# Performance work log

Measured on AMD Instinct MI355X. Metric: run time of the kernel, lower is better.

## Reference

```python
import jax, jax.numpy as jnp
import numpy as np

HIDDEN = 1024
N_HEADS = 16
HEAD_DIM = HIDDEN // N_HEADS  # 64
B, N = 2, 2048
SCALE = HIDDEN ** (-0.5)  # NOTE: original scales by full hidden_size, not head_dim


def setup_inputs() -> dict:
    key = jax.random.key(0)
    k1, k2 = jax.random.split(key)
    hidden_states = jax.random.normal(k1, (B, N, HIDDEN), dtype=jnp.float32)
    attention_mask = jnp.ones((B, N), dtype=jnp.int32)
    # per-head no-bias Linear(hidden -> 3*head_dim), stacked: [h, hidden, 3*head_dim]
    W_qkv = jax.random.normal(k2, (N_HEADS, HIDDEN, 3 * HEAD_DIM), dtype=jnp.float32) * (HIDDEN ** -0.5)
    return {"hidden_states": hidden_states, "attention_mask": attention_mask, "W_qkv": W_qkv}


def reference(hidden_states, attention_mask, W_qkv):
    # qkv: [b, h, n, 3*d]
    qkv = jnp.einsum('bnD,hDe->bhne', hidden_states, W_qkv)
    q, k, v = jnp.split(qkv, 3, axis=-1)  # each [b, h, n, d]
    scores = jnp.einsum('bhid,bhjd->bhij', q, k) * SCALE
    mask = attention_mask[:, None, None, :] == 0  # [b,1,1,n]
    scores = jnp.where(mask, -jnp.inf, scores)
    attn = jax.nn.softmax(scores, axis=-1)
    out = jnp.einsum('bhij,bhjd->bhid', attn, v)  # [b, h, n, d]
    # rearrange 'b h n d -> b n (h d)'
    return jnp.transpose(out, (0, 2, 1, 3)).reshape(out.shape[0], out.shape[2], -1)
```

## Files before the change

### kernel.cpp

```cpp
#include <hip/hip_runtime.h>
#include <hip/hip_bf16.h>


#define NH   16
#define HD   64
#define SEQ  2048
#define HID  1024
#define E3   192
#define QSCALE 0.04508422017f
#define MBIAS  -43.2808512f

typedef __attribute__((ext_vector_type(8))) short short8;
typedef __attribute__((ext_vector_type(4))) float f32x4;
typedef __attribute__((ext_vector_type(16))) float f32x16;
typedef unsigned short ushort_t;

#define MFMA16(a, b, c) __builtin_amdgcn_mfma_f32_16x16x32_bf16((a), (b), (c), 0, 0, 0)
#define MFMA32(a, b, c) __builtin_amdgcn_mfma_f32_32x32x16_bf16((a), (b), (c), 0, 0, 0)

#if __has_builtin(__builtin_amdgcn_exp2f)
#define EXP2(x) __builtin_amdgcn_exp2f(x)
#else
#define EXP2(x) exp2f(x)
#endif

static __device__ __forceinline__ ushort_t f2bf(float x) {
    unsigned u = __builtin_bit_cast(unsigned, x);
    unsigned r = u + 0x7fff + ((u >> 16) & 1);
    return (ushort_t)(r >> 16);
}

static __device__ __forceinline__ unsigned pack_trunc(float hi, float lo) {
#if __has_builtin(__builtin_amdgcn_perm)
    return __builtin_amdgcn_perm(__builtin_bit_cast(unsigned, hi),
                                 __builtin_bit_cast(unsigned, lo), 0x07060302u);
#else
    return (__builtin_bit_cast(unsigned, hi) & 0xffff0000u) |
           (__builtin_bit_cast(unsigned, lo) >> 16);
#endif
}

static __device__ __forceinline__ void load_lds16(const void* g, void* l) {
    __builtin_amdgcn_global_load_lds(
        (__attribute__((address_space(1))) void*)(g),
        (__attribute__((address_space(3))) void*)(l), 16, 0, 0);
}

__global__ __launch_bounds__(256) void k_cvt(const void* __restrict__ Xv,
                                             const void* __restrict__ Wv,
                                             ushort_t* __restrict__ Xb,
                                             ushort_t* __restrict__ Wt,
                                             int* __restrict__ flagp) {
    __shared__ int cnt;
    __shared__ ushort_t tile[64][72];
    const int t = threadIdx.x;
    if (threadIdx.x == 0) cnt = 0;
    __syncthreads();

    if (blockIdx.x < 1024) {
        const unsigned* X32 = (const unsigned*)Xv;
        if (t < 64) {
            unsigned u = X32[(size_t)blockIdx.x * 2048 + t * 32 + 7];
            int bexp = (u >> 7) & 0xFF;
            if (bexp >= 0x68 && bexp <= 0x90) atomicAdd(&cnt, 1);
        }
        __syncthreads();
        const int isf32 = (cnt < 32);
        if (blockIdx.x == 0 && t == 0) *flagp = isf32;

        const size_t base = ((size_t)blockIdx.x * 256 + t) * 16;
        if (isf32) {
            const float* Xf = (const float*)Xv;
            ushort_t tmp[16];
#pragma unroll
            for (int c = 0; c < 4; ++c) {
                float4 v = *(const float4*)(Xf + base + c * 4);
                tmp[c * 4 + 0] = f2bf(v.x); tmp[c * 4 + 1] = f2bf(v.y);
                tmp[c * 4 + 2] = f2bf(v.z); tmp[c * 4 + 3] = f2bf(v.w);
            }
            *(float4*)(Xb + base)     = ((const float4*)tmp)[0];
            *(float4*)(Xb + base + 8) = ((const float4*)tmp)[1];
        } else {
            const ushort_t* Xh = (const ushort_t*)Xv;
            *(float4*)(Xb + base)     = *(const float4*)(Xh + base);
            *(float4*)(Xb + base + 8) = *(const float4*)(Xh + base + 8);
        }
    } else {
        const int wb = blockIdx.x - 1024;
        const unsigned* W32 = (const unsigned*)Wv;
        if (t < 64) {
            unsigned u = W32[(size_t)wb * 2048 + t * 32 + 7];
            int bexp = (u >> 7) & 0xFF;
            if (bexp >= 0x68 && bexp <= 0x90) atomicAdd(&cnt, 1);
        }
        __syncthreads();
        const int isf32 = (cnt < 32);

        const int h  = wb & 15;
        const int dt = (wb >> 4) & 15;
        const int et = wb >> 8;
        const int D0 = dt * 64, e0 = et * 64;
#pragma unroll
        for (int r = 0; r < 2; ++r) {
            int row = r * 32 + (t >> 3);
            int col = (t & 7) * 8;
            size_t base = ((size_t)(h * HID + D0 + row)) * E3 + e0 + col;
            if (isf32) {
                const float* Wf = (const float*)Wv;
                float4 a = *(const float4*)(Wf + base);
                float4 c = *(const float4*)(Wf + base + 4);
                tile[row][col + 0] = f2bf(a.x); tile[row][col + 1] = f2bf(a.y);
                tile[row][col + 2] = f2bf(a.z); tile[row][col + 3] = f2bf(a.w);
                tile[row][col + 4] = f2bf(c.x); tile[row][col + 5] = f2bf(c.y);
                tile[row][col + 6] = f2bf(c.z); tile[row][col + 7] = f2bf(c.w);
            } else {
                *(float4*)&tile[row][col] = *(const float4*)((const ushort_t*)Wv + base);
            }
        }
        __syncthreads();
#pragma unroll
        for (int r = 0; r < 2; ++r) {
            int erow = r * 32 + (t >> 3);
            int dcol = (t & 7) * 8;
            ushort_t vals[8];
#pragma unroll
            for (int i = 0; i < 8; ++i) vals[i] = tile[dcol + i][erow];
            *(float4*)(Wt + ((size_t)(h * E3 + e0 + erow)) * HID + D0 + dcol) = *(float4*)vals;
        }
    }
}

__global__ __launch_bounds__(256) void k_qkv(const ushort_t* __restrict__ Xb,
                                             const ushort_t* __restrict__ Wt,
                                             ushort_t* __restrict__ Qb,
                                             ushort_t* __restrict__ Kb,
                                             ushort_t* __restrict__ Vtb) {
    __shared__ __align__(16) ushort_t smem[2 * 128 * 64];
    ushort_t* Xl = smem;
    ushort_t* Wl = smem + 128 * 64;

    const int bid = blockIdx.y * 24 + blockIdx.x;
    const int xcd = bid & 7, pos = bid >> 3;
    const int e0 = (xcd * 3 + (pos >> 5)) * 128;
    const int m0 = (pos & 31) * 128;
    const int b  = m0 >> 11;
    const int n0 = m0 & 2047;
    const int t = threadIdx.x;
    const int w = t >> 6, lane = t & 63, l15 = lane & 15, quad = lane >> 4;
    const int wrow0 = (w & 1) * 64, wcol0 = (w >> 1) * 64;
    const int srow = lane >> 3;
    const int scb  = (lane & 7) ^ srow;

    f32x4 acc[4][4];
#pragma unroll
    for (int i = 0; i < 4; ++i)
#pragma unroll
        for (int j = 0; j < 4; ++j) acc[i][j] = (f32x4){0.f, 0.f, 0.f, 0.f};

    for (int k0 = 0; k0 < HID; k0 += 64) {
        __syncthreads();
#pragma unroll
        for (int cc = 0; cc < 4; ++cc) {
            const int ch  = w * 4 + cc;
            const int row = ch * 8 + srow;
            load_lds16(Xb + (size_t)(m0 + row) * HID + k0 + scb * 8, &Xl[ch * 512]);
            load_lds16(Wt + (size_t)(e0 + row) * HID + k0 + scb * 8, &Wl[ch * 512]);
        }
        __syncthreads();
#pragma unroll
        for (int kh = 0; kh < 2; ++kh) {
            short8 af[4], bfm[4];
#pragma unroll
            for (int i = 0; i < 4; ++i) {
                const int r = wrow0 + i * 16 + l15;
                af[i] = *(const short8*)&Xl[r * 64 + ((kh * 4 + quad) ^ (r & 7)) * 8];
            }
#pragma unroll
            for (int j = 0; j < 4; ++j) {
                const int r = wcol0 + j * 16 + l15;
                bfm[j] = *(const short8*)&Wl[r * 64 + ((kh * 4 + quad) ^ (r & 7)) * 8];
            }
#pragma unroll
            for (int i = 0; i < 4; ++i)
#pragma unroll
                for (int j = 0; j < 4; ++j)
                    acc[i][j] = MFMA16(af[i], bfm[j], acc[i][j]);
        }
    }

    __syncthreads();
#pragma unroll
    for (int p = 0; p < 2; ++p) {
        const int E0  = e0 + p * 64;
        const int hh  = E0 / 192;
        const int r0p = E0 - hh * 192;
        const int own = ((w >> 1) == p);
        if (r0p < 128) {
            if (own) {
                const float sc = (r0p == 0) ? QSCALE : 1.0f;
#pragma unroll
                for (int i = 0; i < 4; ++i)
#pragma unroll
                    for (int j = 0; j < 4; ++j)
#pragma unroll
                        for (int reg = 0; reg < 4; ++reg)
                            smem[(wrow0 + i * 16 + quad * 4 + reg) * 72 + j * 16 + l15] =
                                f2bf(acc[i][j][reg] * sc);
            }
            __syncthreads();
            ushort_t* dstb = (r0p == 0) ? Qb : Kb;
            const int r = t >> 1, part = t & 1;
            size_t dst = ((size_t)(b * NH + hh) * SEQ + n0 + r) * HD + part * 32;
#pragma unroll
            for (int c = 0; c < 4; ++c)
                *(float4*)(dstb + dst + c * 8) = *(const float4*)&smem[r * 72 + part * 32 + c * 8];
        } else {
            if (own) {
#pragma unroll
                for (int i = 0; i < 4; ++i)
#pragma unroll
                    for (int j = 0; j < 4; ++j)
#pragma unroll
                        for (int reg = 0; reg < 4; ++reg)
                            smem[(j * 16 + l15) * 136 + wrow0 + i * 16 + quad * 4 + reg] =
                                f2bf(acc[i][j][reg]);
            }
            __syncthreads();
            const int dr = t >> 2, part = t & 3;
            size_t dst = ((size_t)(b * NH + hh) * HD + dr) * SEQ + n0 + part * 32;
#pragma unroll
            for (int c = 0; c < 4; ++c)
                *(float4*)(Vtb + dst + c * 8) = *(const float4*)&smem[dr * 136 + part * 32 + c * 8];
        }
        if (p == 0) __syncthreads();
    }
}


#define SMPACK(sv, h0v, h1v)                                                  \
    {                                                                         \
        _Pragma("unroll")                                                     \
        for (int g = 0; g < 4; ++g) {                                         \
            float p0 = EXP2(sv[4*g+0]); float p1 = EXP2(sv[4*g+1]);           \
            float p2 = EXP2(sv[4*g+2]); float p3 = EXP2(sv[4*g+3]);           \
            l_r += (p0 + p1) + (p2 + p3);                                     \
            unsigned a0 = pack_trunc(p1, p0), a1 = pack_trunc(p3, p2);        \
            unsigned b0 = a0, b1 = a1;                                        \
            asm volatile("v_permlane32_swap_b32 %0, %1" : "+v"(a0), "+v"(b0));\
            asm volatile("v_permlane32_swap_b32 %0, %1" : "+v"(a1), "+v"(b1));\
            h0v[g*2+0] = a0; h1v[g*2+0] = b0;                                 \
            h0v[g*2+1] = a1; h1v[g*2+1] = b1;                                 \
        }                                                                     \
    }

#define MAKE_PB(dst, h0v, h1v, GB)                                            \
    {                                                                         \
        unsigned w0_ = hi ? h0v[(GB+1)*2+0] : h0v[(GB)*2+0];                  \
        unsigned w1_ = hi ? h0v[(GB+1)*2+1] : h0v[(GB)*2+1];                  \
        unsigned w2_ = hi ? h1v[(GB+1)*2+0] : h1v[(GB)*2+0];                  \
        unsigned w3_ = hi ? h1v[(GB+1)*2+1] : h1v[(GB)*2+1];                  \
        uint4 u_ = {w0_, w1_, w2_, w3_};                                      \
        dst = __builtin_bit_cast(short8, u_);                                 \
    }

__global__ __launch_bounds__(512, 4) void k_attn(const ushort_t* __restrict__ Qb,
                                                 const ushort_t* __restrict__ Kb,
                                                 const ushort_t* __restrict__ Vtb,
                                                 const int* __restrict__ mask,
                                                 void* __restrict__ outv,
                                                 const int* __restrict__ flagp) {
    __shared__ __align__(16) char smem_raw[73728];
    float* biasl = (float*)(smem_raw + 65536);

    const int isf32 = *flagp;
    const int bidl = blockIdx.y * 16 + blockIdx.x;
    const int xcd8 = bidl & 7, posx = bidl >> 3;
    const int bh   = xcd8 * 4 + (posx >> 4);
    const int q0   = (posx & 15) * 128;
    const int b  = bh >> 4, h = bh & 15;
    const int t  = threadIdx.x;
    const int w  = t >> 6, lane = t & 63;
    const int wq = w >> 1, jh = w & 1;
    const int c31 = lane & 31, hi = lane >> 5;
    const int srow8 = lane >> 3;
    const int scb   = (lane & 7) ^ srow8;
    const int vrow4 = lane >> 4;
    const int vb15  = lane & 15;
    const int rx7   = c31 & 7;
    const int rx15  = c31 & 15;

    {
        ushort_t* kb = (ushort_t*)(smem_raw);
        ushort_t* vb = (ushort_t*)(smem_raw + 16384);
#pragma unroll
        for (int c = 0; c < 2; ++c) {
            const int krow = w * 16 + c * 8 + srow8;
            load_lds16(Kb + ((size_t)bh * SEQ + krow) * HD + scb * 8,
                       &kb[(w * 2 + c) * 512]);
            const int vrow = w * 8 + c * 4 + vrow4;
            load_lds16(Vtb + ((size_t)bh * HD + vrow) * SEQ + ((vb15 ^ (vrow & 15)) * 8),
                       &vb[(w * 2 + c) * 512]);
        }
    }

    int lm = 0;
    for (int i = t; i < SEQ; i += 512) {
        int mv = mask[b * SEQ + i];
        biasl[i] = mv ? 0.0f : MBIAS;
        lm |= (mv == 0);
    }
    const int qrow = q0 + wq * 32 + c31;
    short8 qB[4];
#pragma unroll
    for (int ds = 0; ds < 4; ++ds)
        qB[ds] = *(const short8*)(Qb + ((size_t)bh * SEQ + qrow) * HD + ds * 16 + hi * 8);

    const int use_bias = __syncthreads_or(lm);

    const f32x16 z16 = {0.f,0.f,0.f,0.f,0.f,0.f,0.f,0.f,0.f,0.f,0.f,0.f,0.f,0.f,0.f,0.f};
    f32x16 oa = z16, ob = z16;
    float l_r = 0.f;

    for (int j0 = 0; j0 < SEQ; j0 += 128) {
        const int idx = (j0 >> 7) & 1;
        asm volatile("s_waitcnt vmcnt(0)" ::: "memory");
        __builtin_amdgcn_s_barrier();
        asm volatile("" ::: "memory");
        if (j0 + 128 < SEQ) {
            ushort_t* kb2 = (ushort_t*)(smem_raw + (idx ^ 1) * 32768);
            ushort_t* vb2 = kb2 + 8192;
#pragma unroll
            for (int c = 0; c < 2; ++c) {
                const int krow = w * 16 + c * 8 + srow8;
                load_lds16(Kb + ((size_t)bh * SEQ + j0 + 128 + krow) * HD + scb * 8,
                           &kb2[(w * 2 + c) * 512]);
                const int vrow = w * 8 + c * 4 + vrow4;
                load_lds16(Vtb + ((size_t)bh * HD + vrow) * SEQ + j0 + 128 + ((vb15 ^ (vrow & 15)) * 8),
                           &vb2[(w * 2 + c) * 512]);
            }
        }
        ushort_t* kb = (ushort_t*)(smem_raw + idx * 32768);
        ushort_t* vb = kb + 8192;

        const int jr0 = jh * 64 + c31;
        const int jr1 = jh * 64 + 32 + c31;
        f32x16 s0, s1;
        __builtin_amdgcn_s_setprio(1);
#pragma unroll
        for (int ds = 0; ds < 4; ++ds) {
            short8 kf0 = *(const short8*)&kb[jr0 * 64 + (((2 * ds + hi) ^ rx7) * 8)];
            short8 kf1 = *(const short8*)&kb[jr1 * 64 + (((2 * ds + hi) ^ rx7) * 8)];
            s0 = MFMA32(kf0, qB[ds], ds ? s0 : z16);
            s1 = MFMA32(kf1, qB[ds], ds ? s1 : z16);
        }
        __builtin_amdgcn_s_setprio(0);
        if (use_bias) {
#pragma unroll
            for (int g = 0; g < 4; ++g) {
                float4 bj0 = *(const float4*)&biasl[j0 + jh * 64 + 8 * g + 4 * hi];
                float4 bj1 = *(const float4*)&biasl[j0 + jh * 64 + 32 + 8 * g + 4 * hi];
                s0[4*g+0] += bj0.x; s0[4*g+1] += bj0.y; s0[4*g+2] += bj0.z; s0[4*g+3] += bj0.w;
                s1[4*g+0] += bj1.x; s1[4*g+1] += bj1.y; s1[4*g+2] += bj1.z; s1[4*g+3] += bj1.w;
            }
        }

        unsigned h0a[8], h1a[8], h0b[8], h1b[8];
        SMPACK(s0, h0a, h1a);
        SMPACK(s1, h0b, h1b);

        __builtin_amdgcn_s_setprio(1);
#pragma unroll
        for (int half = 0; half < 2; ++half) {
#pragma unroll
            for (int c13 = 0; c13 < 2; ++c13) {
                short8 pb;
                if (half == 0) { MAKE_PB(pb, h0a, h1a, 2 * c13); }
                else           { MAKE_PB(pb, h0b, h1b, 2 * c13); }
                const int pblk = (jh * 4 + half * 2 + c13) * 2 + hi;
                short8 va0 = *(const short8*)&vb[(c31)      * 128 + ((pblk ^ rx15) * 8)];
                short8 va1 = *(const short8*)&vb[(32 + c31) * 128 + ((pblk ^ rx15) * 8)];
                oa = MFMA32(va0, pb, oa);
                ob = MFMA32(va1, pb, ob);
            }
        }
        __builtin_amdgcn_s_setprio(0);
    }

    float l_h = l_r + __shfl_xor(l_r, 32);

    __syncthreads();
    float* Obuf = (float*)smem_raw;
    float* Lbuf = (float*)(smem_raw + 65536);
    const int slot = (wq * 64 + lane) * 36;
    if (jh == 1) {
#pragma unroll
        for (int g = 0; g < 4; ++g) {
            *(float4*)&Obuf[slot + g * 4]      = (float4){oa[4*g], oa[4*g+1], oa[4*g+2], oa[4*g+3]};
            *(float4*)&Obuf[slot + 16 + g * 4] = (float4){ob[4*g], ob[4*g+1], ob[4*g+2], ob[4*g+3]};
        }
        Lbuf[wq * 64 + lane] = l_h;
    }
    __syncthreads();
    float rinv = 0.f;
    if (jh == 0) {
        const float l_tot = l_h + Lbuf[wq * 64 + lane];
        rinv = 1.0f / l_tot;
#pragma unroll
        for (int g = 0; g < 4; ++g) {
            float4 pa = *(const float4*)&Obuf[slot + g * 4];
            float4 pb4 = *(const float4*)&Obuf[slot + 16 + g * 4];
            oa[4*g] += pa.x; oa[4*g+1] += pa.y; oa[4*g+2] += pa.z; oa[4*g+3] += pa.w;
            ob[4*g] += pb4.x; ob[4*g+1] += pb4.y; ob[4*g+2] += pb4.z; ob[4*g+3] += pb4.w;
        }
    }
    __syncthreads();

    const int qlr = wq * 32 + c31;
    const int r = t >> 2, part = t & 3;
    if (!isf32) {
        ushort_t* Ol = (ushort_t*)smem_raw;
        if (jh == 0) {
#pragma unroll
            for (int dt = 0; dt < 2; ++dt) {
                const f32x16 ov = dt ? ob : oa;
#pragma unroll
                for (int g = 0; g < 4; ++g) {
                    const int d0 = dt * 32 + 8 * g + 4 * hi;
                    uint2 u;
                    u.x = (unsigned)f2bf(ov[4*g+0] * rinv) | ((unsigned)f2bf(ov[4*g+1] * rinv) << 16);
                    u.y = (unsigned)f2bf(ov[4*g+2] * rinv) | ((unsigned)f2bf(ov[4*g+3] * rinv) << 16);
                    *(uint2*)&Ol[qlr * 72 + d0] = u;
                }
            }
        }
        __syncthreads();
        ushort_t* outp = (ushort_t*)outv;
        size_t dst = ((size_t)b * SEQ + q0 + r) * HID + h * HD + part * 16;
        float4 v0 = *(const float4*)&Ol[r * 72 + part * 16];
        float4 v1 = *(const float4*)&Ol[r * 72 + part * 16 + 8];
        *(float4*)(outp + dst)     = v0;
        *(float4*)(outp + dst + 8) = v1;
    } else {
        float* Olf = (float*)smem_raw;
        if (jh == 0) {
#pragma unroll
            for (int dt = 0; dt < 2; ++dt) {
                const f32x16 ov = dt ? ob : oa;
#pragma unroll
                for (int g = 0; g < 4; ++g) {
                    const int d0 = dt * 32 + 8 * g + 4 * hi;
                    float4 fv;
                    fv.x = ov[4*g+0] * rinv; fv.y = ov[4*g+1] * rinv;
                    fv.z = ov[4*g+2] * rinv; fv.w = ov[4*g+3] * rinv;
                    *(float4*)&Olf[qlr * 68 + d0] = fv;
                }
            }
        }
        __syncthreads();
        float* outp = (float*)outv;
        size_t dst = ((size_t)b * SEQ + q0 + r) * HID + h * HD + part * 16;
#pragma unroll
        for (int c = 0; c < 4; ++c) {
            float4 v = *(const float4*)&Olf[r * 68 + part * 16 + c * 4];
            *(float4*)(outp + dst + c * 4) = v;
        }
    }
}

extern "C" void kernel_launch(void* const* d_in, const int* in_sizes, int n_in,
                              void* d_out, int out_size, void* d_ws, size_t ws_size,
                              hipStream_t stream) {
    const void* X    = d_in[0];
    const int*  mask = (const int*)d_in[1];
    const void* W    = d_in[2];

    char* ws = (char*)d_ws;
    ushort_t* Qb    = (ushort_t*)(ws);
    ushort_t* Kb    = (ushort_t*)(ws + 8388608);
    ushort_t* Vtb   = (ushort_t*)(ws + 16777216);
    ushort_t* Wtb   = (ushort_t*)(ws + 25165824);
    int*      flagp = (int*)(ws + 31457280);
    ushort_t* Xb    = (ushort_t*)d_out;

    k_cvt<<<1792, 256, 0, stream>>>(X, W, Xb, Wtb, flagp);
    k_qkv<<<dim3(24, 32), 256, 0, stream>>>(Xb, Wtb, Qb, Kb, Vtb);
    k_attn<<<dim3(16, 32), 512, 0, stream>>>(Qb, Kb, Vtb, mask, d_out, flagp);
}
```

Measured before the change: 179.0 us.

## Switch QKV projection to 32x32 MFMA tiles and drop setprio hints in attention

The QKV projection GEMM now computes each wave's 64x64 tile with four 32x32x16 bf16 MFMAs per k-step instead of sixteen 16x16x32 MFMAs. That cuts LDS fragment reads per k-slice from eight to four per lane, and the epilogue scatter is rewritten for the 32x32 accumulator layout. Separately, the s_setprio raise/lower around the attention MFMA sections is removed, which changes wave scheduling priority in the flash-attention loop. The larger accumulator tiles may change register pressure and issue behaviour.

```diff
diff --git a/kernel.cpp b/kernel.cpp
--- a/kernel.cpp
+++ b/kernel.cpp
@@ -15,7 +15,6 @@
 typedef __attribute__((ext_vector_type(16))) float f32x16;
 typedef unsigned short ushort_t;
 
-#define MFMA16(a, b, c) __builtin_amdgcn_mfma_f32_16x16x32_bf16((a), (b), (c), 0, 0, 0)
 #define MFMA32(a, b, c) __builtin_amdgcn_mfma_f32_32x32x16_bf16((a), (b), (c), 0, 0, 0)
 
 #if __has_builtin(__builtin_amdgcn_exp2f)
@@ -146,16 +145,22 @@
     const int b  = m0 >> 11;
     const int n0 = m0 & 2047;
     const int t = threadIdx.x;
-    const int w = t >> 6, lane = t & 63, l15 = lane & 15, quad = lane >> 4;
+    const int w = t >> 6, lane = t & 63;
+    const int c31 = lane & 31, hi = lane >> 5;
     const int wrow0 = (w & 1) * 64, wcol0 = (w >> 1) * 64;
     const int srow = lane >> 3;
     const int scb  = (lane & 7) ^ srow;
 
-    f32x4 acc[4][4];
-#pragma unroll
-    for (int i = 0; i < 4; ++i)
-#pragma unroll
-        for (int j = 0; j < 4; ++j) acc[i][j] = (f32x4){0.f, 0.f, 0.f, 0.f};
+    f32x16 acc[2][2];
+#pragma unroll
+    for (int mi = 0; mi < 2; ++mi)
+#pragma unroll
+        for (int ni = 0; ni < 2; ++ni)
+#pragma unroll
+            for (int r = 0; r < 16; ++r) acc[mi][ni][r] = 0.f;
+
+    const int ra = wrow0 + c31,      rb = wrow0 + 32 + c31;
+    const int rc = wcol0 + c31,      rd = wcol0 + 32 + c31;
 
     for (int k0 = 0; k0 < HID; k0 += 64) {
         __syncthreads();
@@ -168,23 +173,16 @@
         }
         __syncthreads();
 #pragma unroll
-        for (int kh = 0; kh < 2; ++kh) {
-            short8 af[4], bfm[4];
-#pragma unroll
-            for (int i = 0; i < 4; ++i) {
-                const int r = wrow0 + i * 16 + l15;
-                af[i] = *(const short8*)&Xl[r * 64 + ((kh * 4 + quad) ^ (r & 7)) * 8];
-            }
-#pragma unroll
-            for (int j = 0; j < 4; ++j) {
-                const int r = wcol0 + j * 16 + l15;
-                bfm[j] = *(const short8*)&Wl[r * 64 + ((kh * 4 + quad) ^ (r & 7)) * 8];
-            }
-#pragma unroll
-            for (int i = 0; i < 4; ++i)
-#pragma unroll
-                for (int j = 0; j < 4; ++j)
-                    acc[i][j] = MFMA16(af[i], bfm[j], acc[i][j]);
+        for (int ds = 0; ds < 4; ++ds) {
+            const int blk = 2 * ds + hi;
+            short8 af0 = *(const short8*)&Xl[ra * 64 + ((blk ^ (ra & 7)) * 8)];
+            short8 af1 = *(const short8*)&Xl[rb * 64 + ((blk ^ (rb & 7)) * 8)];
+            short8 bf0 = *(const short8*)&Wl[rc * 64 + ((blk ^ (rc & 7)) * 8)];
+            short8 bf1 = *(const short8*)&Wl[rd * 64 + ((blk ^ (rd & 7)) * 8)];
+            acc[0][0] = MFMA32(af0, bf0, acc[0][0]);
+            acc[0][1] = MFMA32(af0, bf1, acc[0][1]);
+            acc[1][0] = MFMA32(af1, bf0, acc[1][0]);
+            acc[1][1] = MFMA32(af1, bf1, acc[1][1]);
         }
     }
 
@@ -199,13 +197,14 @@
             if (own) {
                 const float sc = (r0p == 0) ? QSCALE : 1.0f;
 #pragma unroll
-                for (int i = 0; i < 4; ++i)
-#pragma unroll
-                    for (int j = 0; j < 4; ++j)
-#pragma unroll
-                        for (int reg = 0; reg < 4; ++reg)
-                            smem[(wrow0 + i * 16 + quad * 4 + reg) * 72 + j * 16 + l15] =
-                                f2bf(acc[i][j][reg] * sc);
+                for (int mi = 0; mi < 2; ++mi)
+#pragma unroll
+                    for (int ni = 0; ni < 2; ++ni)
+#pragma unroll
+                        for (int reg = 0; reg < 16; ++reg) {
+                            const int m_loc = wrow0 + mi * 32 + (reg & 3) + 8 * (reg >> 2) + 4 * hi;
+                            smem[m_loc * 72 + ni * 32 + c31] = f2bf(acc[mi][ni][reg] * sc);
+                        }
             }
             __syncthreads();
             ushort_t* dstb = (r0p == 0) ? Qb : Kb;
@@ -217,13 +216,15 @@
         } else {
             if (own) {
 #pragma unroll
-                for (int i = 0; i < 4; ++i)
-#pragma unroll
-                    for (int j = 0; j < 4; ++j)
-#pragma unroll
-                        for (int reg = 0; reg < 4; ++reg)
-                            smem[(j * 16 + l15) * 136 + wrow0 + i * 16 + quad * 4 + reg] =
-                                f2bf(acc[i][j][reg]);
+                for (int mi = 0; mi < 2; ++mi)
+#pragma unroll
+                    for (int ni = 0; ni < 2; ++ni)
+#pragma unroll
+                        for (int reg = 0; reg < 16; ++reg) {
+                            const int d  = ni * 32 + c31;
+                            const int nl = wrow0 + mi * 32 + (reg & 3) + 8 * (reg >> 2) + 4 * hi;
+                            smem[d * 136 + nl] = f2bf(acc[mi][ni][reg]);
+                        }
             }
             __syncthreads();
             const int dr = t >> 2, part = t & 3;
@@ -345,7 +346,6 @@
         const int jr0 = jh * 64 + c31;
         const int jr1 = jh * 64 + 32 + c31;
         f32x16 s0, s1;
-        __builtin_amdgcn_s_setprio(1);
 #pragma unroll
         for (int ds = 0; ds < 4; ++ds) {
             short8 kf0 = *(const short8*)&kb[jr0 * 64 + (((2 * ds + hi) ^ rx7) * 8)];
@@ -353,7 +353,6 @@
             s0 = MFMA32(kf0, qB[ds], ds ? s0 : z16);
             s1 = MFMA32(kf1, qB[ds], ds ? s1 : z16);
         }
-        __builtin_amdgcn_s_setprio(0);
         if (use_bias) {
 #pragma unroll
             for (int g = 0; g < 4; ++g) {
@@ -368,7 +367,6 @@
         SMPACK(s0, h0a, h1a);
         SMPACK(s1, h0b, h1b);
 
-        __builtin_amdgcn_s_setprio(1);
 #pragma unroll
         for (int half = 0; half < 2; ++half) {
 #pragma unroll
@@ -383,7 +381,6 @@
                 ob = MFMA32(va1, pb, ob);
             }
         }
-        __builtin_amdgcn_s_setprio(0);
     }
 
     float l_h = l_r + __shfl_xor(l_r, 32);
```

New measurement: 178.8 us. No clear change (-0.1%).
